# Optimization experiments

Hardware: AMD Instinct MI355X
Metric: run time of the kernel (lower is better)

Reference implementation:

```python
import jax, jax.numpy as jnp
from jax import lax
import numpy as np

# Guide bandwidths (sigma^2) for the cross-bilateral weights.
SIGMA_ALBEDO = 0.01
SIGMA_NORMAL = 0.1
SIGMA_DEPTH = 0.1
EPS = 1e-10

B, H, W = 4, 720, 1280
WIN = 11


def setup_inputs() -> dict:
    key = jax.random.key(0)
    k1, k2, k3, k4 = jax.random.split(key, 4)
    inp = jax.random.normal(k1, (B, 3, H, W), dtype=jnp.float32)
    albedo = jax.random.uniform(k2, (B, 3, H, W), dtype=jnp.float32)
    normal = jax.random.normal(k3, (B, 3, H, W), dtype=jnp.float32)
    normal = normal / (jnp.linalg.norm(normal, axis=1, keepdims=True) + EPS)
    depth = jax.random.uniform(k4, (B, 1, H, W), dtype=jnp.float32)
    return {"input": inp, "albedo": albedo, "normal": normal,
            "depth": depth, "win_size": WIN}


def _cross_bilateral(inp, albedo, normal, depth, win_size):
    pad = win_size // 2
    b, c, h, w = inp.shape

    def pad4(x):
        return jnp.pad(x, ((0, 0), (0, 0), (pad, pad), (pad, pad)), mode="edge")

    ip, ap, np_, dp = pad4(inp), pad4(albedo), pad4(normal), pad4(depth)

    # All (dy, dx) taps in the window, scanned to keep memory O(B*C*H*W).
    offs = jnp.asarray([(dy, dx) for dy in range(win_size) for dx in range(win_size)],
                       dtype=jnp.int32)

    def tap(carry, off):
        acc, wsum = carry
        dy, dx = off[0], off[1]

        def sl(x):
            return lax.dynamic_slice(x, (0, 0, dy, dx), (b, x.shape[1], h, w))

        dA = jnp.sum((albedo - sl(ap)) ** 2, axis=1, keepdims=True)  # [B,1,H,W]
        dN = jnp.sum((normal - sl(np_)) ** 2, axis=1, keepdims=True)
        dD = (depth - sl(dp)) ** 2
        wgt = jnp.exp(-(dA / SIGMA_ALBEDO + dN / SIGMA_NORMAL + dD / SIGMA_DEPTH))
        return (acc + wgt * sl(ip), wsum + wgt), None

    init = (jnp.zeros_like(inp), jnp.zeros((b, 1, h, w), dtype=inp.dtype))
    (acc, wsum), _ = lax.scan(tap, init, offs)
    return acc / jnp.maximum(wsum, EPS)


def reference(input, albedo, normal, depth, win_size):
    return _cross_bilateral(input, albedo, normal, depth, win_size)
```

## Files before the change

kernel.cpp:

```cpp
#include <hip/hip_runtime.h>
#include <math.h>


#define HH   720
#define WW   1280
#define PAD  5
#define WIN  11
#define TW   16
#define TH   16
#define HLO  26

typedef _Float16 h2 __attribute__((ext_vector_type(2)));

__device__ __forceinline__ unsigned pkh(_Float16 a, _Float16 b) {
    unsigned lo = __builtin_bit_cast(unsigned short, a);
    unsigned hi = __builtin_bit_cast(unsigned short, b);
    return lo | (hi << 16);
}
__device__ __forceinline__ h2 bch2(unsigned u) { return __builtin_bit_cast(h2, u); }

__global__ __launch_bounds__(256, 8)
void xbilateral_kernel(const float* __restrict__ inp,
                       const float* __restrict__ alb,
                       const float* __restrict__ nrm,
                       const float* __restrict__ dep,
                       float* __restrict__ out)
{
    __shared__ uint4 sG [HLO][HLO];
    __shared__ float sGG[HLO][HLO];
    __shared__ uint2 sI [HLO][HLO];

    const int tid = threadIdx.x;
    const int lx  = tid & 15;
    const int ly  = tid >> 4;
    const int bx0 = blockIdx.x * TW;
    const int by0 = blockIdx.y * TH;
    const int b   = blockIdx.z;

    const float kA2 = 16.98653137f;
    const float kN2 = 5.37154913f;

    const size_t plane = (size_t)HH * WW;
    const float* albB = alb + (size_t)b * 3 * plane;
    const float* nrmB = nrm + (size_t)b * 3 * plane;
    const float* inpB = inp + (size_t)b * 3 * plane;
    const float* depB = dep + (size_t)b * plane;

    for (int idx = tid; idx < HLO * HLO; idx += 256) {
        int r = idx / HLO;
        int c = idx - r * HLO;
        int gy = by0 + r - PAD; gy = min(max(gy, 0), HH - 1);
        int gx = bx0 + c - PAD; gx = min(max(gx, 0), WW - 1);
        size_t o = (size_t)gy * WW + gx;
        _Float16 u0 = (_Float16)(albB[o] * kA2);
        _Float16 u1 = (_Float16)(albB[plane + o] * kA2);
        _Float16 u2 = (_Float16)(albB[2 * plane + o] * kA2);
        _Float16 u3 = (_Float16)(depB[o] * kN2);
        _Float16 u4 = (_Float16)(nrmB[o] * kN2);
        _Float16 u5 = (_Float16)(nrmB[plane + o] * kN2);
        _Float16 u6 = (_Float16)(nrmB[2 * plane + o] * kN2);
        float f0 = (float)u0, f1 = (float)u1, f2 = (float)u2, f3 = (float)u3;
        float f4 = (float)u4, f5 = (float)u5, f6 = (float)u6;
        sG[r][c]  = make_uint4(pkh(u0, u1), pkh(u2, u3), pkh(u4, u5), pkh(u6, (_Float16)0.f));
        sGG[r][c] = 0.5f * (f0 * f0 + f1 * f1 + f2 * f2 + f3 * f3 +
                            f4 * f4 + f5 * f5 + f6 * f6);
        _Float16 i0 = (_Float16)inpB[o];
        _Float16 i1 = (_Float16)inpB[plane + o];
        _Float16 i2 = (_Float16)inpB[2 * plane + o];
        sI[r][c] = make_uint2(pkh(i0, i1), pkh(i2, (_Float16)1.f));
    }
    __syncthreads();

    uint4 gc = sG[ly + PAD][lx + PAD];
    h2 c0 = bch2(gc.x), c1 = bch2(gc.y), c2 = bch2(gc.z), c3 = bch2(gc.w);
    float nggp = -sGG[ly + PAD][lx + PAD];

    float4 acc = make_float4(0.f, 0.f, 0.f, 0.f);

#pragma unroll 1
    for (int wy = 0; wy < WIN; ++wy) {
        const uint4* rg  = &sG [ly + wy][lx];
        const float* rgg = &sGG[ly + wy][lx];
        const uint2* ri  = &sI [ly + wy][lx];
#pragma unroll
        for (int dx = 0; dx < WIN; ++dx) {
            uint4 g = rg[dx];
            float s = nggp - rgg[dx];
            uint2 t = ri[dx];
            h2 g0 = bch2(g.x), g1 = bch2(g.y), g2 = bch2(g.z), g3 = bch2(g.w);
            s = fmaf((float)g0.x, (float)c0.x, s);
            s = fmaf((float)g0.y, (float)c0.y, s);
            s = fmaf((float)g1.x, (float)c1.x, s);
            s = fmaf((float)g1.y, (float)c1.y, s);
            s = fmaf((float)g2.x, (float)c2.x, s);
            s = fmaf((float)g2.y, (float)c2.y, s);
            s = fmaf((float)g3.x, (float)c3.x, s);
            float w = __builtin_amdgcn_exp2f(s);
            h2 i01 = bch2(t.x), i2o = bch2(t.y);
            acc.x = fmaf(w, (float)i01.x, acc.x);
            acc.y = fmaf(w, (float)i01.y, acc.y);
            acc.z = fmaf(w, (float)i2o.x, acc.z);
            acc.w += w;
        }
    }

    const int ox = bx0 + lx;
    const int oy = by0 + ly;
    float* outB = out + (size_t)b * 3 * plane;
    float inv = 1.0f / fmaxf(acc.w, 1e-10f);
    size_t o = (size_t)oy * WW + ox;
    outB[o]             = acc.x * inv;
    outB[plane + o]     = acc.y * inv;
    outB[2 * plane + o] = acc.z * inv;
}

extern "C" void kernel_launch(void* const* d_in, const int* in_sizes, int n_in,
                              void* d_out, int out_size, void* d_ws, size_t ws_size,
                              hipStream_t stream) {
    const float* inp = (const float*)d_in[0];
    const float* alb = (const float*)d_in[1];
    const float* nrm = (const float*)d_in[2];
    const float* dep = (const float*)d_in[3];
    float* out = (float*)d_out;

    dim3 grid(WW / TW, HH / TH, 4);
    dim3 block(256);
    xbilateral_kernel<<<grid, block, 0, stream>>>(inp, alb, nrm, dep, out);
}
```

Measured before the change: 262.9 us.

## Compute three vertical outputs per thread to reuse shared-memory tap loads

Each thread now produces three vertically adjacent output pixels, so every shared-memory row load feeds up to three output computations. The loop runs over 13 rows and masks out-of-window taps by subtracting a large constant from the exponent. The tile grows to 32x24 with a larger halo, which cuts the halo overhead per output. In exchange there are more registers per thread, occupancy drops to 4 blocks, and 2 of the 39 computed taps per row are wasted exp work.

```diff
diff --git a/kernel.cpp b/kernel.cpp
--- a/kernel.cpp
+++ b/kernel.cpp
@@ -6,9 +6,11 @@
 #define WW   1280
 #define PAD  5
 #define WIN  11
-#define TW   16
-#define TH   16
-#define HLO  26
+#define TW   32
+#define TH   24
+#define HR   34
+#define HC   42
+#define BIGE 1.0e4f
 
 typedef _Float16 h2 __attribute__((ext_vector_type(2)));
 
@@ -19,20 +21,20 @@
 }
 __device__ __forceinline__ h2 bch2(unsigned u) { return __builtin_bit_cast(h2, u); }
 
-__global__ __launch_bounds__(256, 8)
+__global__ __launch_bounds__(256, 4)
 void xbilateral_kernel(const float* __restrict__ inp,
                        const float* __restrict__ alb,
                        const float* __restrict__ nrm,
                        const float* __restrict__ dep,
                        float* __restrict__ out)
 {
-    __shared__ uint4 sG [HLO][HLO];
-    __shared__ float sGG[HLO][HLO];
-    __shared__ uint2 sI [HLO][HLO];
+    __shared__ uint4 sG [HR][HC];
+    __shared__ float sGG[HR][HC];
+    __shared__ uint2 sI [HR][HC];
 
     const int tid = threadIdx.x;
-    const int lx  = tid & 15;
-    const int ly  = tid >> 4;
+    const int lx  = tid & 31;
+    const int ly  = tid >> 5;
     const int bx0 = blockIdx.x * TW;
     const int by0 = blockIdx.y * TH;
     const int b   = blockIdx.z;
@@ -46,9 +48,9 @@
     const float* inpB = inp + (size_t)b * 3 * plane;
     const float* depB = dep + (size_t)b * plane;
 
-    for (int idx = tid; idx < HLO * HLO; idx += 256) {
-        int r = idx / HLO;
-        int c = idx - r * HLO;
+    for (int idx = tid; idx < HR * HC; idx += 256) {
+        int r = idx / HC;
+        int c = idx - r * HC;
         int gy = by0 + r - PAD; gy = min(max(gy, 0), HH - 1);
         int gx = bx0 + c - PAD; gx = min(max(gx, 0), WW - 1);
         size_t o = (size_t)gy * WW + gx;
@@ -71,47 +73,76 @@
     }
     __syncthreads();
 
-    uint4 gc = sG[ly + PAD][lx + PAD];
-    h2 c0 = bch2(gc.x), c1 = bch2(gc.y), c2 = bch2(gc.z), c3 = bch2(gc.w);
-    float nggp = -sGG[ly + PAD][lx + PAD];
+    const int py0 = 3 * ly;
 
-    float4 acc = make_float4(0.f, 0.f, 0.f, 0.f);
+    uint4 gA = sG[py0 + 0 + PAD][lx + PAD];
+    uint4 gB = sG[py0 + 1 + PAD][lx + PAD];
+    uint4 gC = sG[py0 + 2 + PAD][lx + PAD];
+    h2 cA0 = bch2(gA.x), cA1 = bch2(gA.y), cA2 = bch2(gA.z), cA3 = bch2(gA.w);
+    h2 cB0 = bch2(gB.x), cB1 = bch2(gB.y), cB2 = bch2(gB.z), cB3 = bch2(gB.w);
+    h2 cC0 = bch2(gC.x), cC1 = bch2(gC.y), cC2 = bch2(gC.z), cC3 = bch2(gC.w);
+    float ncA = -sGG[py0 + 0 + PAD][lx + PAD];
+    float ncB = -sGG[py0 + 1 + PAD][lx + PAD];
+    float ncC = -sGG[py0 + 2 + PAD][lx + PAD];
+
+    float4 aA = make_float4(0.f, 0.f, 0.f, 0.f);
+    float4 aB = make_float4(0.f, 0.f, 0.f, 0.f);
+    float4 aC = make_float4(0.f, 0.f, 0.f, 0.f);
 
 #pragma unroll 1
-    for (int wy = 0; wy < WIN; ++wy) {
-        const uint4* rg  = &sG [ly + wy][lx];
-        const float* rgg = &sGG[ly + wy][lx];
-        const uint2* ri  = &sI [ly + wy][lx];
+    for (int wy = 0; wy < 13; ++wy) {
+        float baseA = ncA - ((wy <= 10) ? 0.f : BIGE);
+        float baseB = ncB - (((unsigned)(wy - 1) <= 10u) ? 0.f : BIGE);
+        float baseC = ncC - ((wy >= 2) ? 0.f : BIGE);
+
+        const uint4* pG  = &sG [py0 + wy][lx];
+        const float* pGG = &sGG[py0 + wy][lx];
+        const uint2* pI  = &sI [py0 + wy][lx];
+
 #pragma unroll
         for (int dx = 0; dx < WIN; ++dx) {
-            uint4 g = rg[dx];
-            float s = nggp - rgg[dx];
-            uint2 t = ri[dx];
+            uint4 g  = pG[dx];
+            float gt = pGG[dx];
+            uint2 ti = pI[dx];
             h2 g0 = bch2(g.x), g1 = bch2(g.y), g2 = bch2(g.z), g3 = bch2(g.w);
-            s = fmaf((float)g0.x, (float)c0.x, s);
-            s = fmaf((float)g0.y, (float)c0.y, s);
-            s = fmaf((float)g1.x, (float)c1.x, s);
-            s = fmaf((float)g1.y, (float)c1.y, s);
-            s = fmaf((float)g2.x, (float)c2.x, s);
-            s = fmaf((float)g2.y, (float)c2.y, s);
-            s = fmaf((float)g3.x, (float)c3.x, s);
-            float w = __builtin_amdgcn_exp2f(s);
-            h2 i01 = bch2(t.x), i2o = bch2(t.y);
-            acc.x = fmaf(w, (float)i01.x, acc.x);
-            acc.y = fmaf(w, (float)i01.y, acc.y);
-            acc.z = fmaf(w, (float)i2o.x, acc.z);
-            acc.w += w;
+            h2 i01 = bch2(ti.x), i2o = bch2(ti.y);
+
+#define TAP(S, C0, C1, C2, C3, ACC)                                            \
+            {                                                                   \
+                float s = (S) - gt;                                             \
+                s = fmaf((float)g0.x, (float)C0.x, s);                          \
+                s = fmaf((float)g0.y, (float)C0.y, s);                          \
+                s = fmaf((float)g1.x, (float)C1.x, s);                          \
+                s = fmaf((float)g1.y, (float)C1.y, s);                          \
+                s = fmaf((float)g2.x, (float)C2.x, s);                          \
+                s = fmaf((float)g2.y, (float)C2.y, s);                          \
+                s = fmaf((float)g3.x, (float)C3.x, s);                          \
+                float w = __builtin_amdgcn_exp2f(s);                            \
+                ACC.x = fmaf(w, (float)i01.x, ACC.x);                           \
+                ACC.y = fmaf(w, (float)i01.y, ACC.y);                           \
+                ACC.z = fmaf(w, (float)i2o.x, ACC.z);                           \
+                ACC.w += w;                                                     \
+            }
+            TAP(baseA, cA0, cA1, cA2, cA3, aA)
+            TAP(baseB, cB0, cB1, cB2, cB3, aB)
+            TAP(baseC, cC0, cC1, cC2, cC3, aC)
+#undef TAP
         }
     }
 
     const int ox = bx0 + lx;
-    const int oy = by0 + ly;
     float* outB = out + (size_t)b * 3 * plane;
-    float inv = 1.0f / fmaxf(acc.w, 1e-10f);
-    size_t o = (size_t)oy * WW + ox;
-    outB[o]             = acc.x * inv;
-    outB[plane + o]     = acc.y * inv;
-    outB[2 * plane + o] = acc.z * inv;
+#define WOUT(K, ACC)                                                            \
+    {                                                                           \
+        int oy = by0 + py0 + K;                                                 \
+        float inv = 1.0f / fmaxf(ACC.w, 1e-10f);                                \
+        size_t o = (size_t)oy * WW + ox;                                        \
+        outB[o]             = ACC.x * inv;                                      \
+        outB[plane + o]     = ACC.y * inv;                                      \
+        outB[2 * plane + o] = ACC.z * inv;                                      \
+    }
+    WOUT(0, aA) WOUT(1, aB) WOUT(2, aC)
+#undef WOUT
 }
 
 extern "C" void kernel_launch(void* const* d_in, const int* in_sizes, int n_in,
```

Result: faster. 257.2 us (-2.2%).
